# Performance work log

Hardware: AMD Instinct MI355X
Metric: run time of the kernel (lower is better)

The kernel has to match this reference:

```python
import jax, jax.numpy as jnp
import numpy as np

B, L, E, H = 2, 2048, 1024, 16
HD = E // H


def _rel_shift(x):
    # x: [b, h, q, k] -> Transformer-XL relative shift via pad+reshape trick
    b, h, q, k = x.shape
    xp = jnp.pad(x, ((0, 0), (0, 0), (0, 0), (1, 0)))  # pad left of last dim
    xp = xp.reshape(b, h, k + 1, q)
    return xp[:, :, 1:, :].reshape(b, h, q, k)


def setup_inputs() -> dict:
    key = jax.random.key(0)
    ks = jax.random.split(key, 16)
    s = 0.02
    return {
        "query": jax.random.normal(ks[0], (B, L, E), jnp.float32),
        "key": jax.random.normal(ks[1], (B, L, E), jnp.float32),
        "value": jax.random.normal(ks[2], (B, L, E), jnp.float32),
        "pos_embedding": jax.random.normal(ks[3], (B, L, E), jnp.float32),
        "Wq": jax.random.normal(ks[4], (E, E), jnp.float32) * s,
        "bq": jnp.zeros((E,), jnp.float32),
        "Wk": jax.random.normal(ks[5], (E, E), jnp.float32) * s,
        "bk": jnp.zeros((E,), jnp.float32),
        "Wv": jax.random.normal(ks[6], (E, E), jnp.float32) * s,
        "bv": jnp.zeros((E,), jnp.float32),
        "Wp": jax.random.normal(ks[7], (E, E), jnp.float32) * s,  # Pos linear, no bias
        "Wo": jax.random.normal(ks[8], (E, E), jnp.float32) * s,
        "bo": jnp.zeros((E,), jnp.float32),
        "U": jax.random.normal(ks[9], (H, HD), jnp.float32) * s,
        "V": jax.random.normal(ks[10], (H, HD), jnp.float32) * s,
    }


def reference(query, key, value, pos_embedding, Wq, bq, Wk, bk, Wv, bv, Wp, Wo, bo, U, V):
    b, qlen, e = query.shape
    h, hd = U.shape
    scale = jnp.sqrt(jnp.asarray(e, query.dtype))
    # torch Linear: y = x @ W.T + b
    q = (query @ Wq.T + bq).reshape(b, qlen, h, hd)
    k = (key @ Wk.T + bk).reshape(b, key.shape[1], h, hd)
    v = (value @ Wv.T + bv).reshape(b, value.shape[1], h, hd)
    r = (pos_embedding @ Wp.T).reshape(b, -1, h, hd)
    content_score = jnp.einsum("bqhd,bkhd->bhqk", q + U, k)
    position_score = jnp.einsum("bqhd,bkhd->bhqk", q + V, r)
    position_score = _rel_shift(position_score)
    attention_score = (content_score + position_score) / scale
    # NOTE: the original module applies NO softmax; faithful reproduction.
    # einsum 'bhqk,bvhd->bqhd' sums over both k (scores) and v (values).
    alpha = jnp.einsum("bhqk,bvhd->bqhd", attention_score, v).reshape(b, qlen, e)
    return alpha @ Wo.T + bo
```

## Files before the change

### kernel.cpp

```cpp
#include <hip/hip_runtime.h>

#define BB 2
#define LL 2048
#define EE 1024
#define HH 16
#define HDD 64

typedef __bf16 bf16x8 __attribute__((ext_vector_type(8)));
typedef float f32x4 __attribute__((ext_vector_type(4)));

__device__ __forceinline__ unsigned short f2bf(float f) {
  unsigned int x = __float_as_uint(f);
  return (unsigned short)((x + 0x7FFFu + ((x >> 16) & 1u)) >> 16);
}

__device__ __forceinline__ float bf2f(unsigned short u) {
  return __uint_as_float((unsigned int)u << 16);
}

__device__ __forceinline__ void load_lds16(const void* g, void* l) {
  __builtin_amdgcn_global_load_lds(
      (const __attribute__((address_space(1))) void*)g,
      (__attribute__((address_space(3))) void*)l, 16, 0, 0);
}

#define SUMKV_BLOCKS 256
#define CAST_BLOCKS 1280
#define CAST_STRIDE (CAST_BLOCKS * 256)
__global__ __launch_bounds__(256) void prelude_kernel(
    const float* __restrict__ q, const float* __restrict__ pe,
    const float* __restrict__ wq, const float* __restrict__ wp,
    unsigned short* __restrict__ q16, unsigned short* __restrict__ pe16,
    unsigned short* __restrict__ wq16, unsigned short* __restrict__ wp16,
    const float* __restrict__ key, const float* __restrict__ value,
    float* __restrict__ keysum, float* __restrict__ valsum) {
  if (blockIdx.x < SUMKV_BLOCKS) {
    int blk2 = blockIdx.x;
    int b = blk2 >> 7, ch = blk2 & 127;
    int tid = threadIdx.x;
    const float4* k4 = (const float4*)(key   + ((size_t)b * LL + ch * 16) * EE);
    const float4* v4 = (const float4*)(value + ((size_t)b * LL + ch * 16) * EE);
    float4 ak = make_float4(0.f, 0.f, 0.f, 0.f);
    float4 av = make_float4(0.f, 0.f, 0.f, 0.f);
#pragma unroll 8
    for (int i = 0; i < 16; i++) {
      float4 kk = k4[i * 256 + tid];
      float4 vv = v4[i * 256 + tid];
      ak.x += kk.x; ak.y += kk.y; ak.z += kk.z; ak.w += kk.w;
      av.x += vv.x; av.y += vv.y; av.z += vv.z; av.w += vv.w;
    }
    int e = tid * 4;
    atomicAdd(&keysum[b * EE + e + 0], ak.x);
    atomicAdd(&keysum[b * EE + e + 1], ak.y);
    atomicAdd(&keysum[b * EE + e + 2], ak.z);
    atomicAdd(&keysum[b * EE + e + 3], ak.w);
    atomicAdd(&valsum[b * EE + e + 0], av.x);
    atomicAdd(&valsum[b * EE + e + 1], av.y);
    atomicAdd(&valsum[b * EE + e + 2], av.z);
    atomicAdd(&valsum[b * EE + e + 3], av.w);
  } else {
    const int NQ4 = BB * LL * EE / 4;
    const int NW4 = EE * EE / 4;
    int t = (blockIdx.x - SUMKV_BLOCKS) * 256 + threadIdx.x;
    float4 v[8]; unsigned short* dst[8]; int off[8];
#pragma unroll
    for (int k = 0; k < 8; k++) {
      int i = t + k * CAST_STRIDE;
      const float* src;
      if (i < NQ4)                { src = q;  dst[k] = q16;  off[k] = i; }
      else if (i < 2 * NQ4)       { src = pe; dst[k] = pe16; off[k] = i - NQ4; }
      else if (i < 2 * NQ4 + NW4) { src = wq; dst[k] = wq16; off[k] = i - 2 * NQ4; }
      else                        { src = wp; dst[k] = wp16; off[k] = i - 2 * NQ4 - NW4; }
      v[k] = ((const float4*)src)[off[k]];
    }
#pragma unroll
    for (int k = 0; k < 8; k++) {
      ushort4 u;
      u.x = f2bf(v[k].x); u.y = f2bf(v[k].y); u.z = f2bf(v[k].z); u.w = f2bf(v[k].w);
      ((ushort4*)dst[k])[off[k]] = u;
    }
  }
}

__global__ __launch_bounds__(256) void proj_kernel(
    const float* __restrict__ keysum, const float* __restrict__ valsum,
    const float* __restrict__ Wk, const float* __restrict__ bk,
    const float* __restrict__ Wv, const float* __restrict__ bv,
    float* __restrict__ Kproj, float* __restrict__ Vproj) {
  int wv = threadIdx.x >> 6, lane = threadIdx.x & 63;
  int idx = blockIdx.x * 4 + wv;
  int b = idx >> 10, ep = idx & (EE - 1);
  const float* sum  = blockIdx.z ? valsum : keysum;
  const float* W    = blockIdx.z ? Wv : Wk;
  const float* bias = blockIdx.z ? bv : bk;
  float* outp       = blockIdx.z ? Vproj : Kproj;
  float acc = 0.f;
  for (int k = lane; k < EE; k += 64) acc += sum[b * EE + k] * W[ep * EE + k];
  for (int off = 32; off; off >>= 1) acc += __shfl_down(acc, off, 64);
  if (lane == 0) outp[b * EE + ep] = acc + (float)LL * bias[ep];
}

__global__ __launch_bounds__(256) void gemm_kernel(
    const unsigned short* __restrict__ q16, const unsigned short* __restrict__ wq16,
    const float* __restrict__ bq, unsigned short* __restrict__ qout,
    const unsigned short* __restrict__ pe16, const unsigned short* __restrict__ wp16,
    unsigned short* __restrict__ rout, float* __restrict__ chunks,
    const float* __restrict__ Vproj, const float* __restrict__ Wo,
    float* __restrict__ W2) {
  const int tid = threadIdx.x;
  const int lane = tid & 63;
  const int wv = tid >> 6;

  if (blockIdx.z == 2) {
    int bid = blockIdx.x + 32 * blockIdx.y;
    int wslot = bid * 4 + wv;
    int base = wslot * 32;
    int b = base >> 14;
    int h = (base >> 10) & (HH - 1);
    int e0 = base & (EE - 1);
    float vp = Vproj[b * EE + h * HDD + lane];
    const float* wo = Wo + (size_t)e0 * EE + h * HDD + lane;
    for (int r = 0; r < 32; r++) {
      float acc = vp * wo[(size_t)r * EE];
      for (int off = 32; off; off >>= 1) acc += __shfl_down(acc, off, 64);
      if (lane == 0) W2[((size_t)b * HH + h) * EE + e0 + r] = acc;
    }
    return;
  }

  const int K = EE, N = EE;
  const unsigned short* X; const unsigned short* W; const float* bias;
  unsigned short* Out;
  if (blockIdx.z == 0) { X = q16;  W = wq16; bias = bq;      Out = qout; }
  else                 { X = pe16; W = wp16; bias = nullptr; Out = rout; }

  __shared__ __align__(16) unsigned short As[128 * 32];
  __shared__ __align__(16) unsigned short Bs[128 * 32];

  const int wr = wv >> 1, wc = wv & 1;
  const int m0 = blockIdx.x * 128;
  const int n0 = blockIdx.y * 128;

  const int srow = wv * 16 + (lane >> 2);
  const int scol = (lane & 3) * 8;
  const unsigned short* gA = X + (size_t)(m0 + srow) * K + scol;
  const unsigned short* gB = W + (size_t)(n0 + srow) * K + scol;
  unsigned short* sA = As + wv * 512;
  unsigned short* sB = Bs + wv * 512;

  f32x4 acc[4][4];
#pragma unroll
  for (int i = 0; i < 4; i++)
#pragma unroll
    for (int j = 0; j < 4; j++) acc[i][j] = (f32x4)0.0f;

  const int arow = wr * 64 + (lane & 15);
  const int brow = wc * 64 + (lane & 15);
  const int koff = (lane >> 4) * 8;

  for (int kk = 0; kk < K; kk += 32) {
    load_lds16(gA + kk,                   sA);
    load_lds16(gA + kk + (size_t)64 * K,  sA + 2048);
    load_lds16(gB + kk,                   sB);
    load_lds16(gB + kk + (size_t)64 * K,  sB + 2048);
    __syncthreads();
    bf16x8 af[4], bf[4];
#pragma unroll
    for (int i = 0; i < 4; i++) af[i] = *(const bf16x8*)&As[(arow + i * 16) * 32 + koff];
#pragma unroll
    for (int j = 0; j < 4; j++) bf[j] = *(const bf16x8*)&Bs[(brow + j * 16) * 32 + koff];
#pragma unroll
    for (int i = 0; i < 4; i++)
#pragma unroll
      for (int j = 0; j < 4; j++)
        acc[i][j] = __builtin_amdgcn_mfma_f32_16x16x32_bf16(af[i], bf[j], acc[i][j], 0, 0, 0);
    __syncthreads();
  }

  const int rbase = m0 + wr * 64 + (lane >> 4) * 4;
  const int cbase = n0 + wc * 64 + (lane & 15);
#pragma unroll
  for (int i = 0; i < 4; i++) {
#pragma unroll
    for (int j = 0; j < 4; j++) {
      int col = cbase + j * 16;
      float badd = bias ? bias[col] : 0.f;
#pragma unroll
      for (int g = 0; g < 4; g++) {
        int row = rbase + i * 16 + g;
        Out[(size_t)row * N + col] = f2bf(acc[i][j][g] + badd);
      }
    }
  }

  if (blockIdx.z == 1) {
    int b = m0 >> 11;
    int ch0 = ((m0 & (LL - 1)) >> 5) + wr * 2;
#pragma unroll
    for (int cp = 0; cp < 2; cp++) {
#pragma unroll
      for (int j = 0; j < 4; j++) {
        float s = 0.f;
#pragma unroll
        for (int i = cp * 2; i < cp * 2 + 2; i++)
#pragma unroll
          for (int g = 0; g < 4; g++) s += acc[i][j][g];
        s += __shfl_down(s, 32, 64);
        s += __shfl_down(s, 16, 64);
        if (lane < 16) {
          int col = n0 + wc * 64 + j * 16 + lane;
          chunks[((size_t)b * 64 + ch0 + cp) * EE + col] = s;
        }
      }
    }
  }
}

__global__ __launch_bounds__(256) void scan2f_kernel(
    const unsigned short* __restrict__ qbuf, const unsigned short* __restrict__ rbuf,
    const float* __restrict__ chunks, const float* __restrict__ Kproj,
    const float* __restrict__ U, const float* __restrict__ V,
    float* __restrict__ S1, float* __restrict__ Dbuf) {
  int tid = threadIdx.x, lane = tid & 63;
  int hg = blockIdx.x, ch = blockIdx.y, b = blockIdx.z;
  int e = hg * 256 + tid;
  int h = hg * 4 + (tid >> 6);
  float pre = 0.f, tot = 0.f;
  for (int c = 0; c < 64; c++) {
    float cs = chunks[((size_t)b * 64 + c) * EE + e];
    tot += cs;
    if (c < ch) pre += cs;
  }
  float kp = Kproj[b * EE + e], Ue = U[e], Ve = V[e];
  float run = pre;
  size_t hoff = ((size_t)b * HH + h) * LL;
#pragma unroll 4
  for (int i = 0; i < 32; i++) {
    int m = ch * 32 + i;
    int p = LL - 1 - m;
    float qv = bf2f(qbuf[((size_t)b * LL + p) * EE + e]);
    float rv = bf2f(rbuf[((size_t)b * LL + m) * EE + e]);
    float tq = qv + Ve;
    float d = tq * run;
    float s = tq * tot + (qv + Ue) * kp;
#pragma unroll
    for (int off = 32; off; off >>= 1) {
      d += __shfl_down(d, off, 64);
      s += __shfl_down(s, off, 64);
    }
    if (lane == 0) { Dbuf[hoff + m] = d; S1[hoff + p] = s; }
    run += rv;
  }
}

__global__ __launch_bounds__(256) void out_kernel(
    const float* __restrict__ S1, const float* __restrict__ Dbuf,
    const float* __restrict__ W2, const float* __restrict__ bo,
    float* __restrict__ out) {
  int row0 = blockIdx.x * 8;
  int b = row0 >> 11, p0 = row0 & (LL - 1);
  int tid = threadIdx.x;
  __shared__ float sh[8][HH];
  if (tid < 128) {
    int rr = tid >> 4, h = tid & 15;
    int p = p0 + rr;
    size_t hoff = ((size_t)b * HH + h) * LL;
    float s1 = S1[hoff + p];
    float d1 = Dbuf[hoff + (LL - 1 - p)];
    float d2 = (p == LL - 1) ? 0.f : Dbuf[hoff + (LL - 2 - p)];
    sh[rr][h] = (s1 - d1 + d2) * (1.f / 32.f);
  }
  float4 w2r[HH];
#pragma unroll
  for (int h = 0; h < HH; h++)
    w2r[h] = ((const float4*)(W2 + ((size_t)b * HH + h) * EE))[tid];
  float4 bo4 = ((const float4*)bo)[tid];
  __syncthreads();
#pragma unroll
  for (int rr = 0; rr < 8; rr++) {
    float4 acc = bo4;
#pragma unroll
    for (int h = 0; h < HH; h++) {
      float s = sh[rr][h];
      acc.x += s * w2r[h].x; acc.y += s * w2r[h].y;
      acc.z += s * w2r[h].z; acc.w += s * w2r[h].w;
    }
    ((float4*)out)[(size_t)(row0 + rr) * 256 + tid] = acc;
  }
}

extern "C" void kernel_launch(void* const* d_in, const int* in_sizes, int n_in,
                              void* d_out, int out_size, void* d_ws, size_t ws_size,
                              hipStream_t stream) {
  const float* query = (const float*)d_in[0];
  const float* key   = (const float*)d_in[1];
  const float* value = (const float*)d_in[2];
  const float* pos   = (const float*)d_in[3];
  const float* Wq = (const float*)d_in[4];
  const float* bq = (const float*)d_in[5];
  const float* Wk = (const float*)d_in[6];
  const float* bk = (const float*)d_in[7];
  const float* Wv = (const float*)d_in[8];
  const float* bv = (const float*)d_in[9];
  const float* Wp = (const float*)d_in[10];
  const float* Wo = (const float*)d_in[11];
  const float* bo = (const float*)d_in[12];
  const float* U  = (const float*)d_in[13];
  const float* V  = (const float*)d_in[14];
  float* out = (float*)d_out;

  char* ws = (char*)d_ws;
  size_t o = 0;
  auto take = [&](size_t bytes) -> char* {
    char* p = ws + o;
    o += (bytes + 255) & ~(size_t)255;
    return p;
  };
  float* keysum = (float*)take(BB * EE * 4);
  float* valsum = (float*)take(BB * EE * 4);
  float* Kproj  = (float*)take(BB * EE * 4);
  float* Vproj  = (float*)take(BB * EE * 4);
  float* W2     = (float*)take((size_t)BB * HH * EE * 4);
  float* S1     = (float*)take((size_t)BB * HH * LL * 4);
  float* Dbuf   = (float*)take((size_t)BB * HH * LL * 4);
  float* chunks = (float*)take((size_t)BB * 64 * EE * 4);
  unsigned short* qbuf = (unsigned short*)take((size_t)BB * LL * EE * 2);
  unsigned short* rbuf = (unsigned short*)take((size_t)BB * LL * EE * 2);
  unsigned short* q16  = (unsigned short*)take((size_t)BB * LL * EE * 2);
  unsigned short* pe16 = (unsigned short*)take((size_t)BB * LL * EE * 2);
  unsigned short* wq16 = (unsigned short*)take((size_t)EE * EE * 2);
  unsigned short* wp16 = (unsigned short*)take((size_t)EE * EE * 2);

  hipMemsetAsync(keysum, 0, (size_t)2 * BB * EE * 4, stream);

  prelude_kernel<<<SUMKV_BLOCKS + CAST_BLOCKS, 256, 0, stream>>>(
      query, pos, Wq, Wp, q16, pe16, wq16, wp16, key, value, keysum, valsum);
  proj_kernel<<<dim3(BB * EE / 4, 1, 2), 256, 0, stream>>>(
      keysum, valsum, Wk, bk, Wv, bv, Kproj, Vproj);
  gemm_kernel<<<dim3(BB * LL / 128, EE / 128, 3), 256, 0, stream>>>(
      q16, wq16, bq, qbuf, pe16, wp16, rbuf, chunks, Vproj, Wo, W2);
  scan2f_kernel<<<dim3(4, 64, BB), 256, 0, stream>>>(qbuf, rbuf, chunks, Kproj, U, V, S1, Dbuf);
  out_kernel<<<dim3(BB * LL / 8), 256, 0, stream>>>(S1, Dbuf, W2, bo, out);
}
```

Baseline: 225.0 us.

## Double-buffer LDS tiles and swizzle layout in the projection GEMM

```diff
diff --git a/kernel.cpp b/kernel.cpp
--- a/kernel.cpp
+++ b/kernel.cpp
@@ -134,19 +134,17 @@
   if (blockIdx.z == 0) { X = q16;  W = wq16; bias = bq;      Out = qout; }
   else                 { X = pe16; W = wp16; bias = nullptr; Out = rout; }
 
-  __shared__ __align__(16) unsigned short As[128 * 32];
-  __shared__ __align__(16) unsigned short Bs[128 * 32];
+  __shared__ __align__(16) unsigned short As[2][128 * 32];
+  __shared__ __align__(16) unsigned short Bs[2][128 * 32];
 
   const int wr = wv >> 1, wc = wv & 1;
   const int m0 = blockIdx.x * 128;
   const int n0 = blockIdx.y * 128;
 
   const int srow = wv * 16 + (lane >> 2);
-  const int scol = (lane & 3) * 8;
-  const unsigned short* gA = X + (size_t)(m0 + srow) * K + scol;
-  const unsigned short* gB = W + (size_t)(n0 + srow) * K + scol;
-  unsigned short* sA = As + wv * 512;
-  unsigned short* sB = Bs + wv * 512;
+  const int s_src = ((lane & 3) - ((lane >> 3) & 3)) & 3;
+  const unsigned short* gA = X + (size_t)(m0 + srow) * K + s_src * 8;
+  const unsigned short* gB = W + (size_t)(n0 + srow) * K + s_src * 8;
 
   f32x4 acc[4][4];
 #pragma unroll
@@ -156,26 +154,37 @@
 
   const int arow = wr * 64 + (lane & 15);
   const int brow = wc * 64 + (lane & 15);
-  const int koff = (lane >> 4) * 8;
-
-  for (int kk = 0; kk < K; kk += 32) {
-    load_lds16(gA + kk,                   sA);
-    load_lds16(gA + kk + (size_t)64 * K,  sA + 2048);
-    load_lds16(gB + kk,                   sB);
-    load_lds16(gB + kk + (size_t)64 * K,  sB + 2048);
-    __syncthreads();
+  const int koff = (((lane >> 4) + ((lane & 15) >> 1)) & 3) * 8;
+
+#define GSTAGE(BI, KK)                                                   \
+  do {                                                                   \
+    load_lds16(gA + (KK),                  &As[BI][wv * 512]);           \
+    load_lds16(gA + (KK) + (size_t)64 * K, &As[BI][wv * 512 + 2048]);    \
+    load_lds16(gB + (KK),                  &Bs[BI][wv * 512]);           \
+    load_lds16(gB + (KK) + (size_t)64 * K, &Bs[BI][wv * 512 + 2048]);    \
+  } while (0)
+
+  GSTAGE(0, 0);
+  __syncthreads();
+  int bi = 0;
+  for (int t = 0; t < K / 32; ++t) {
+    if (t + 1 < K / 32) GSTAGE(bi ^ 1, (t + 1) * 32);
     bf16x8 af[4], bf[4];
 #pragma unroll
-    for (int i = 0; i < 4; i++) af[i] = *(const bf16x8*)&As[(arow + i * 16) * 32 + koff];
-#pragma unroll
-    for (int j = 0; j < 4; j++) bf[j] = *(const bf16x8*)&Bs[(brow + j * 16) * 32 + koff];
+    for (int i = 0; i < 4; i++)
+      af[i] = *(const bf16x8*)&As[bi][(arow + i * 16) * 32 + koff];
+#pragma unroll
+    for (int j = 0; j < 4; j++)
+      bf[j] = *(const bf16x8*)&Bs[bi][(brow + j * 16) * 32 + koff];
 #pragma unroll
     for (int i = 0; i < 4; i++)
 #pragma unroll
       for (int j = 0; j < 4; j++)
         acc[i][j] = __builtin_amdgcn_mfma_f32_16x16x32_bf16(af[i], bf[j], acc[i][j], 0, 0, 0);
     __syncthreads();
-  }
+    bi ^= 1;
+  }
+#undef GSTAGE
 
   const int rbase = m0 + wr * 64 + (lane >> 4) * 4;
   const int cbase = n0 + wc * 64 + (lane & 15);
```

After: 226.5 us. Within noise of the previous version (+0.7%).
